# Kernel optimization log

Measured on AMD Instinct MI355X. Metric: run time of the kernel, lower is better.

## Reference

```python
import jax, jax.numpy as jnp
import numpy as np

B, L, D, H = 2, 2048, 1024, 16
HD = D // H
KW = 4  # conv kernel width


def layernorm(x, g, b, eps=1e-5):
    m = jnp.mean(x, axis=-1, keepdims=True)
    v = jnp.var(x, axis=-1, keepdims=True)
    return (x - m) / jnp.sqrt(v + eps) * g + b


def causal_conv(x, w, b):
    # torch Conv1d(k=4, padding=3, groups=D) then truncate to L => causal depthwise conv
    # out[t] = sum_j w[:, j] * x[t - 3 + j] + b
    xp = jnp.pad(x, ((0, 0), (KW - 1, 0), (0, 0)))
    Lx = x.shape[1]
    out = b
    for j in range(KW):
        out = out + xp[:, j:j + Lx, :] * w[:, j]
    return out


def setup_inputs() -> dict:
    key = jax.random.key(0)
    ks = jax.random.split(key, 16)
    r = lambda i, shape, s=0.02: jax.random.normal(ks[i], shape, jnp.float32) * s
    return dict(
        x=r(0, (B, L, D), 1.0),
        Wqkv=r(1, (D, 3 * D)), Wout=r(2, (D, D)),
        Wgate=r(3, (D, D)), bgate=jnp.zeros((D,), jnp.float32),
        fn_g=jnp.ones((D,), jnp.float32), fn_b=jnp.zeros((D,), jnp.float32),
        dn_g=jnp.ones((D,), jnp.float32), dn_b=jnp.zeros((D,), jnp.float32),
        dWq=r(4, (D, D)), dWk=r(5, (D, D)), dWv=r(6, (D, D)), dWo=r(7, (D, D)),
        Wbeta=r(8, (D, H)), bbeta=jnp.zeros((H,), jnp.float32),
        cq_w=r(9, (D, KW), 0.1), cq_b=jnp.zeros((D,), jnp.float32),
        ck_w=r(10, (D, KW), 0.1), ck_b=jnp.zeros((D,), jnp.float32),
        ln_g=jnp.ones((D,), jnp.float32), ln_b=jnp.zeros((D,), jnp.float32),
    )


def _delta_scan(q, k, v, beta):
    # q,k,v: (B,L,H,HD) ; beta: (B,L,H)
    Bx = q.shape[0]
    S0 = jnp.zeros((Bx, H, HD, HD), q.dtype)
    z0 = jnp.zeros((Bx, H, HD), q.dtype)

    def step(carry, inp):
        S, z = carry
        q_t, k_t, v_t, b_t = inp  # (B,H,HD) x3, (B,H)
        y = jnp.einsum('bhij,bhj->bhi', S, q_t)
        denom = jnp.einsum('bhi,bhi->bh', z, q_t)[..., None] + 1e-6
        y = y / denom
        old = jnp.einsum('bhij,bhj->bhi', S, k_t)
        delta = v_t - old
        S = S + b_t[..., None, None] * jnp.einsum('bhi,bhj->bhij', delta, k_t)
        z = z + b_t[..., None] * k_t
        return (S, z), y

    xs = (jnp.moveaxis(q, 1, 0), jnp.moveaxis(k, 1, 0),
          jnp.moveaxis(v, 1, 0), jnp.moveaxis(beta, 1, 0))
    (S, z), ys = jax.lax.scan(step, (S0, z0), xs)
    return jnp.moveaxis(ys, 0, 1), S, z  # (B,L,H,HD)


def _forward(x, Wqkv, Wout, Wgate, bgate, fn_g, fn_b, dn_g, dn_b,
             dWq, dWk, dWv, dWo, Wbeta, bbeta, cq_w, cq_b, ck_w, ck_b, ln_g, ln_b):
    Bx, Lx, Dx = x.shape
    # ---- flash (full causal, L<=2048 branch) ----
    qkv = (x @ Wqkv).reshape(Bx, Lx, 3, H, HD)
    q = jnp.moveaxis(qkv[:, :, 0], 1, 2)  # (B,H,L,HD)
    k = jnp.moveaxis(qkv[:, :, 1], 1, 2)
    v = jnp.moveaxis(qkv[:, :, 2], 1, 2)
    scale = HD ** -0.5
    scores = jnp.einsum('bhqd,bhkd->bhqk', q, k) * scale
    causal = jnp.tril(jnp.ones((Lx, Lx), bool))
    scores = jnp.where(causal, scores, -jnp.inf)
    attn = jax.nn.softmax(scores, axis=-1)
    flash = jnp.einsum('bhqk,bhkd->bhqd', attn, v)
    flash = jnp.moveaxis(flash, 1, 2).reshape(Bx, Lx, Dx) @ Wout
    flash = layernorm(flash, fn_g, fn_b)
    # ---- delta branch ----
    dq = causal_conv(x @ dWq, cq_w, cq_b).reshape(Bx, Lx, H, HD)
    dk = causal_conv(x @ dWk, ck_w, ck_b).reshape(Bx, Lx, H, HD)
    dv = (x @ dWv).reshape(Bx, Lx, H, HD)
    dk = dk / jnp.maximum(jnp.linalg.norm(dk, axis=-1, keepdims=True), 1e-12)
    beta = jax.nn.sigmoid(x @ Wbeta + bbeta)  # (B,L,H)
    ys, S, z = _delta_scan(dq, dk, dv, beta)
    delta_out = layernorm(ys.reshape(Bx, Lx, Dx) @ dWo, ln_g, ln_b)  # DeltaAttention layer_norm
    delta_out = layernorm(delta_out, dn_g, dn_b)  # hybrid delta_norm
    # ---- gate ----
    gate = jax.nn.sigmoid(x @ Wgate + bgate)
    out = gate * flash + (1.0 - gate) * delta_out
    return out, S, z


def reference(x, Wqkv, Wout, Wgate, bgate, fn_g, fn_b, dn_g, dn_b,
              dWq, dWk, dWv, dWo, Wbeta, bbeta, cq_w, cq_b, ck_w, ck_b, ln_g, ln_b):
    return _forward(x, Wqkv, Wout, Wgate, bgate, fn_g, fn_b, dn_g, dn_b,
                    dWq, dWk, dWv, dWo, Wbeta, bbeta, cq_w, cq_b, ck_w, ck_b, ln_g, ln_b)
```

## Files before the change

### kernel.cpp

```cpp
#include <hip/hip_runtime.h>
#include <hip/hip_bf16.h>

constexpr int B_ = 2, L_ = 2048, D_ = 1024, H_ = 16;

using bf16x8 = __attribute__((ext_vector_type(8))) short;
using f32x4  = __attribute__((ext_vector_type(4))) float;

__device__ __forceinline__ short f2b(float f) {
  union { float f; unsigned int u; } v; v.f = f;
  unsigned int r = (v.u + 0x7FFFu + ((v.u >> 16) & 1u)) >> 16;
  return (short)r;
}
__device__ __forceinline__ float b2f(unsigned short h) {
  union { unsigned int u; float f; } v; v.u = ((unsigned int)h) << 16; return v.f;
}
__device__ __forceinline__ void split2(float x, float y, unsigned int& h, unsigned int& l) {
  unsigned short hx = (unsigned short)f2b(x), hy = (unsigned short)f2b(y);
  h = (unsigned int)hx | ((unsigned int)hy << 16);
  unsigned short lx = (unsigned short)f2b(x - b2f(hx)), ly = (unsigned short)f2b(y - b2f(hy));
  l = (unsigned int)lx | ((unsigned int)ly << 16);
}
__device__ __forceinline__ float dot4(float4 a, float4 b) {
  return a.x * b.x + a.y * b.y + a.z * b.z + a.w * b.w;
}
// ... 116 lines not shown
    bf16x8 af[MT], bf[NT];
#pragma unroll
    for (int mt = 0; mt < MT; ++mt) af[mt] = *(bf16x8*)&As[(wm + mt * 16 + l15) * 32 + quad * 8];
#pragma unroll
    for (int nt = 0; nt < NT; ++nt) bf[nt] = *(bf16x8*)&Bs[(wn + nt * 16 + l15) * 32 + quad * 8];
#pragma unroll
    for (int mt = 0; mt < MT; ++mt)
#pragma unroll
      for (int nt = 0; nt < NT; ++nt)
        acc[mt][nt] = __builtin_amdgcn_mfma_f32_16x16x32_bf16(af[mt], bf[nt], acc[mt][nt], 0, 0, 0);
  }
#pragma unroll
  for (int mt = 0; mt < MT; ++mt)
#pragma unroll
    for (int nt = 0; nt < NT; ++nt)
#pragma unroll
      for (int r = 0; r < 4; ++r) {
        size_t idx = (size_t)(m0 + wm + mt * 16 + quad * 4 + r) * N + n0 + wn + nt * 16 + l15;
        if constexpr (sizeof(CT) == 2) C[idx] = f2b(acc[mt][nt][r]);
        else C[idx] = acc[mt][nt][r];
      }
}

template <int BN>
__global__ __launch_bounds__(256) void gemm_bt(const float* __restrict__ A, const short* __restrict__ Wt,
                                               float* __restrict__ C, int N, int K) {
  gemm_bt_body<BN, float>(A, Wt, C, N, K, blockIdx.x, blockIdx.y);
}

__global__ __launch_bounds__(256) void gemm_bt_h(const float* __restrict__ A, const short* __restrict__ Wt,
                                                 short* __restrict__ C, int N, int K) {
  gemm_bt_body<128, short>(A, Wt, C, N, K, blockIdx.x, blockIdx.y);
}

__global__ __launch_bounds__(256) void gemm_bt2(const float* __restrict__ A, const short* __restrict__ Wt1,
                                                const short* __restrict__ Wt2, float* __restrict__ C1,
                                                float* __restrict__ C2) {
  gemm_bt_body<64, float>(A, blockIdx.z ? Wt2 : Wt1, blockIdx.z ? C2 : C1, 1024, 1024,
                          blockIdx.x, blockIdx.y);
}

__global__ __launch_bounds__(256) void gemm_bt_split2(const float* __restrict__ A,
                                                      const short* __restrict__ Wh1, const short* __restrict__ Wl1,
                                                      const short* __restrict__ Wh2, const short* __restrict__ Wl2,
                                                      float* __restrict__ C1, float* __restrict__ C2) {
  constexpr int K = 1024, N = 1024;
  const short* Wh = blockIdx.z ? Wh2 : Wh1;
  const short* Wl = blockIdx.z ? Wl2 : Wl1;
  float* C = blockIdx.z ? C2 : C1;
  __shared__ __align__(16) short Ash[128 * 32];
  __shared__ __align__(16) short Asl[128 * 32];
  __shared__ __align__(16) short Bsh[64 * 32];
  __shared__ __align__(16) short Bsl[64 * 32];
  int tid = threadIdx.x;
  int wave = tid >> 6, lane = tid & 63, quad = lane >> 4, l15 = lane & 15;
  int m0 = blockIdx.y * 128, n0 = blockIdx.x * 64;
  int wm = wave * 32;
  f32x4 acc[2][4];
#pragma unroll
  for (int mt = 0; mt < 2; ++mt)
#pragma unroll
    for (int nt = 0; nt < 4; ++nt) acc[mt][nt] = (f32x4){0.f, 0.f, 0.f, 0.f};
// ... 35 lines not shown
    }
#pragma unroll
    for (int mt = 0; mt < 2; ++mt)
#pragma unroll
      for (int nt = 0; nt < 4; ++nt) {
        f32x4 a = acc[mt][nt];
        a = __builtin_amdgcn_mfma_f32_16x16x32_bf16(al[mt], bh[nt], a, 0, 0, 0);
        a = __builtin_amdgcn_mfma_f32_16x16x32_bf16(ah[mt], bl[nt], a, 0, 0, 0);
        a = __builtin_amdgcn_mfma_f32_16x16x32_bf16(ah[mt], bh[nt], a, 0, 0, 0);
        acc[mt][nt] = a;
      }
  }
#pragma unroll
  for (int mt = 0; mt < 2; ++mt)
#pragma unroll
    for (int nt = 0; nt < 4; ++nt)
#pragma unroll
      for (int r = 0; r < 4; ++r) {
        size_t idx = (size_t)(m0 + wm + mt * 16 + quad * 4 + r) * N + n0 + nt * 16 + l15;
        C[idx] = acc[mt][nt][r];
      }
}

__global__ __launch_bounds__(256) void attn_mfma(const short* __restrict__ qkv, float* __restrict__ outp) {
  __shared__ __align__(16) short Kl[64 * 64];
  __shared__ __align__(16) short Vt[64 * 64];
  __shared__ __align__(16) short Pl[64 * 64];
  int qb = 31 - blockIdx.x, h = blockIdx.y, b = blockIdx.z;
  int tid = threadIdx.x;
  int wave = tid >> 6, lane = tid & 63;
  int quad = lane >> 4, l15 = lane & 15;
  int qrow = qb * 64 + wave * 16 + l15;
  bf16x8 qf[2];
  {
    const short* qbase = qkv + (size_t)(b * L_ + qrow) * 3072 + h * 64;
#pragma unroll
    for (int s = 0; s < 2; ++s) qf[s] = *(const bf16x8*)(qbase + s * 32 + quad * 8);
  }
  f32x4 Of[4];
  float mrow[4], lrow[4], alpha[4];
#pragma unroll
  for (int dt = 0; dt < 4; ++dt) Of[dt] = (f32x4){0.f, 0.f, 0.f, 0.f};
#pragma unroll
  for (int r = 0; r < 4; ++r) { mrow[r] = -1e30f; lrow[r] = 0.f; }

  for (int kt = 0; kt <= qb; ++kt) {
    __syncthreads();
#pragma unroll
    for (int it = 0; it < 2; ++it) {
      int e8 = tid + it * 256;
      int key = e8 >> 3, g = e8 & 7;
      const short* src = qkv + ((size_t)((b * L_ + kt * 64 + key) * 3) + 1) * 1024 + h * 64 + g * 8;
      *(bf16x8*)&Kl[key * 64 + ((g ^ (key & 7)) << 3)] = *(const bf16x8*)src;
    }
    {
      int key4 = tid >> 4;
      int d4 = tid & 15;
      const short* vsrc = qkv + ((size_t)((b * L_ + kt * 64 + key4 * 4) * 3) + 2) * 1024 + h * 64 + d4 * 4;
      short4 v0 = *(const short4*)vsrc;
      short4 v1 = *(const short4*)(vsrc + 3072);
      short4 v2 = *(const short4*)(vsrc + 6144);
      short4 v3 = *(const short4*)(vsrc + 9216);
      short vr0[4] = {v0.x, v0.y, v0.z, v0.w};
      short vr1[4] = {v1.x, v1.y, v1.z, v1.w};
      short vr2[4] = {v2.x, v2.y, v2.z, v2.w};
      short vr3[4] = {v3.x, v3.y, v3.z, v3.w};
      int kg = key4 >> 1, k7b = (key4 & 1) * 4;
#pragma unroll
      for (int jj = 0; jj < 4; ++jj) {
        int d = d4 * 4 + jj;
        short4 sv;
        sv.x = vr0[jj]; sv.y = vr1[jj]; sv.z = vr2[jj]; sv.w = vr3[jj];
        *(short4*)&Vt[d * 64 + ((kg ^ (d & 7)) << 3) + k7b] = sv;
      }
    }
    __syncthreads();
    f32x4 sc[4];
#pragma unroll
    for (int nt = 0; nt < 4; ++nt) sc[nt] = (f32x4){0.f, 0.f, 0.f, 0.f};
#pragma unroll
    for (int s = 0; s < 2; ++s) {
#pragma unroll
      for (int nt = 0; nt < 4; ++nt) {
        int key = nt * 16 + l15;
        bf16x8 kf = *(bf16x8*)&Kl[key * 64 + (((4 * s + quad) ^ (key & 7)) << 3)];
        sc[nt] = __builtin_amdgcn_mfma_f32_16x16x32_bf16(qf[s], kf, sc[nt], 0, 0, 0);
      }
    }
    bool diag = (kt == qb);
#pragma unroll
    for (int r = 0; r < 4; ++r) {
      float sv[4];
#pragma unroll
      for (int nt = 0; nt < 4; ++nt) {
        float v = sc[nt][r] * 0.125f;
        if (diag && (nt * 16 + l15 > wave * 16 + quad * 4 + r)) v = -1e30f;
        sv[nt] = v;
      }
      float mx = fmaxf(fmaxf(sv[0], sv[1]), fmaxf(sv[2], sv[3]));
      mx = fmaxf(mx, __shfl_xor(mx, 1));
      mx = fmaxf(mx, __shfl_xor(mx, 2));
      mx = fmaxf(mx, __shfl_xor(mx, 4));
      mx = fmaxf(mx, __shfl_xor(mx, 8));
      float mnew = fmaxf(mrow[r], mx);
      float al = __expf(mrow[r] - mnew);
      mrow[r] = mnew;
      alpha[r] = al;
      int prow = wave * 16 + quad * 4 + r;
      int r7 = prow & 7;
      float ps = 0.f;
#pragma unroll
      for (int nt = 0; nt < 4; ++nt) {
        float p = __expf(sv[nt] - mnew);
        ps += p;
        Pl[prow * 64 + ((((nt << 1) + (l15 >> 3)) ^ r7) << 3) + (l15 & 7)] = f2b(p);
      }
      ps += __shfl_xor(ps, 1);
      ps += __shfl_xor(ps, 2);
      ps += __shfl_xor(ps, 4);
      ps += __shfl_xor(ps, 8);
      lrow[r] = lrow[r] * al + ps;
    }
#pragma unroll
    for (int dt = 0; dt < 4; ++dt)
#pragma unroll
      for (int r = 0; r < 4; ++r) Of[dt][r] *= alpha[r];
#pragma unroll
    for (int s = 0; s < 2; ++s) {
      bf16x8 pf = *(bf16x8*)&Pl[(wave * 16 + l15) * 64 + (((4 * s + quad) ^ (l15 & 7)) << 3)];
#pragma unroll
      for (int dt = 0; dt < 4; ++dt) {
        int d = dt * 16 + l15;
        bf16x8 vf = *(bf16x8*)&Vt[d * 64 + (((4 * s + quad) ^ (d & 7)) << 3)];
        Of[dt] = __builtin_amdgcn_mfma_f32_16x16x32_bf16(pf, vf, Of[dt], 0, 0, 0);
      }
    }
  }
#pragma unroll
  for (int r = 0; r < 4; ++r) alpha[r] = 1.f / lrow[r];
  int orow = qb * 64 + wave * 16 + quad * 4;
#pragma unroll
  for (int dt = 0; dt < 4; ++dt)
#pragma unroll
    for (int r = 0; r < 4; ++r)
      outp[(size_t)(b * L_ + orow + r) * 1024 + h * 64 + dt * 16 + l15] = Of[dt][r] * alpha[r];
}

__global__ __launch_bounds__(256) void ln_kernel(float* __restrict__ X, const float* __restrict__ g,
                                                 const float* __restrict__ bb) {
  int row = blockIdx.x, tid = threadIdx.x;
  float* xr = X + (size_t)row * D_;
  float v[4], s = 0.f, ss = 0.f;
#pragma unroll
  for (int i = 0; i < 4; ++i) { v[i] = xr[tid + i * 256]; s += v[i]; ss += v[i] * v[i]; }
#pragma unroll
  for (int off = 32; off; off >>= 1) { s += __shfl_xor(s, off); ss += __shfl_xor(ss, off); }
  __shared__ float rs[4], rss[4];
  if ((tid & 63) == 0) { rs[tid >> 6] = s; rss[tid >> 6] = ss; }
  __syncthreads();
  float S = rs[0] + rs[1] + rs[2] + rs[3];
  float SS = rss[0] + rss[1] + rss[2] + rss[3];
  float mean = S * (1.f / 1024.f);
  float var = SS * (1.f / 1024.f) - mean * mean;
  float inv = rsqrtf(var + 1e-5f);
#pragma unroll
  for (int i = 0; i < 4; ++i) {
    int c = tid + i * 256;
    xr[c] = (v[i] - mean) * inv * g[c] + bb[c];
  }
}

__global__ __launch_bounds__(256) void ln2mix_kernel(const float* __restrict__ X,
                                                     const float* __restrict__ g1, const float* __restrict__ b1,
                                                     const float* __restrict__ g2, const float* __restrict__ b2,
                                                     const float* __restrict__ gpre, const float* __restrict__ bgate,
                                                     const float* __restrict__ fo, float* __restrict__ outp) {
  int row = blockIdx.x, tid = threadIdx.x;
  const float* xr = X + (size_t)row * D_;
  __shared__ float rs[4], rss[4];
  float v[4], s = 0.f, ss = 0.f;
#pragma unroll
  for (int i = 0; i < 4; ++i) { v[i] = xr[tid + i * 256]; s += v[i]; ss += v[i] * v[i]; }
#pragma unroll
  for (int off = 32; off; off >>= 1) { s += __shfl_xor(s, off); ss += __shfl_xor(ss, off); }
  if ((tid & 63) == 0) { rs[tid >> 6] = s; rss[tid >> 6] = ss; }
  __syncthreads();
  float S = rs[0] + rs[1] + rs[2] + rs[3];
  float SS = rss[0] + rss[1] + rss[2] + rss[3];
  float mean = S * (1.f / 1024.f);
  float var = SS * (1.f / 1024.f) - mean * mean;
  float inv = rsqrtf(var + 1e-5f);
  s = 0.f; ss = 0.f;
#pragma unroll
  for (int i = 0; i < 4; ++i) {
    int c = tid + i * 256;
    v[i] = (v[i] - mean) * inv * g1[c] + b1[c];
    s += v[i]; ss += v[i] * v[i];
  }
#pragma unroll
  for (int off = 32; off; off >>= 1) { s += __shfl_xor(s, off); ss += __shfl_xor(ss, off); }
  __syncthreads();
  if ((tid & 63) == 0) { rs[tid >> 6] = s; rss[tid >> 6] = ss; }
  __syncthreads();
  S = rs[0] + rs[1] + rs[2] + rs[3];
  SS = rss[0] + rss[1] + rss[2] + rss[3];
  mean = S * (1.f / 1024.f);
  var = SS * (1.f / 1024.f) - mean * mean;
  inv = rsqrtf(var + 1e-5f);
#pragma unroll
  for (int i = 0; i < 4; ++i) {
    int c = tid + i * 256;
    size_t idx = (size_t)row * D_ + c;
    float w = (v[i] - mean) * inv * g2[c] + b2[c];
    float gg = 1.f / (1.f + __expf(-(gpre[idx] + bgate[c])));
    outp[idx] = gg * fo[idx] + (1.f - gg) * w;
  }
}

__global__ __launch_bounds__(256) void convnorm_kernel(const float* __restrict__ qin, const float* __restrict__ kin,
                                                       const float* __restrict__ qw, const float* __restrict__ qb,
                                                       const float* __restrict__ kw, const float* __restrict__ kb,
                                                       float* __restrict__ qout, float* __restrict__ kout) {
  int path = blockIdx.y;
  int row = blockIdx.x * 4 + (threadIdx.x >> 6);
  int lane = threadIdx.x & 63;
  int bl = row >> 4, h = row & 15;
  int t = bl & (L_ - 1);
  int d = h * 64 + lane;
  size_t idx = (size_t)bl * D_ + d;
  const float* xin = path ? kin : qin;
  const float* w = path ? kw : qw;
  const float* bias = path ? kb : qb;
  float acc = bias[d];
#pragma unroll
  for (int j = 0; j < 4; ++j) {
    int tt = t - 3 + j;
    if (tt >= 0) acc += w[d * 4 + j] * xin[idx + (size_t)(j - 3) * D_];
  }
// ... 112 lines not shown
      float4 x2 = *(float4*)&Xl[(u4 * 4 + 2) * 36 + s4];
      float4 x3 = *(float4*)&Xl[(u4 * 4 + 3) * 36 + s4];
      acc.x += bq.x * x0.x + bq.y * x1.x + bq.z * x2.x + bq.w * x3.x;
      acc.y += bq.x * x0.y + bq.y * x1.y + bq.z * x2.y + bq.w * x3.y;
      acc.z += bq.x * x0.z + bq.y * x1.z + bq.z * x2.z + bq.w * x3.z;
      acc.w += bq.x * x0.w + bq.y * x1.w + bq.z * x2.w + bq.w * x3.w;
    }
    *(float4*)&BqM_g[cb * 1024 + tt * 32 + s4] = acc;
  }
  if (tid < 32) {
    float a = 0.f;
#pragma unroll
    for (int s4i = 0; s4i < 8; ++s4i)
      a += dot4(*(float4*)&Bql[tid * 36 + s4i * 4], *(float4*)&bl[s4i * 4]);
    denB_g[cb * 32 + tid] = a;
  }
  if (tid >= 64 && tid < 128) {
    int j = tid - 64;
    float a = 0.f;
#pragma unroll
    for (int s = 0; s < 32; ++s) a += bl[s] * Kl[s * 68 + j];
    zinc_g[cb * 64 + j] = a;
  }
}

__global__ __launch_bounds__(256) void delta_kernel(const float* __restrict__ dq, const float* __restrict__ dk,
                                                    const float* __restrict__ dv, const float* __restrict__ beta,
                                                    const float* __restrict__ MK_g, const float* __restrict__ BqM_g,
                                                    const float* __restrict__ denB_g, const float* __restrict__ zinc_g,
                                                    float* __restrict__ ys, float* __restrict__ outS,
                                                    float* __restrict__ outZ) {
  __shared__ __align__(16) float MKl[2][32 * 68];
  __shared__ __align__(16) float BqMl[2][32 * 36];
  __shared__ __align__(16) float Vl[2][32 * 5];
  __shared__ __align__(16) float bll[2][32];
  __shared__ __align__(16) float dnl[2][32];
  __shared__ __align__(16) float zil[2][64];
  __shared__ __align__(16) float S0l[4 * 68];
  __shared__ __align__(16) float Y0l[32 * 5];
  __shared__ __align__(16) float Rtl[4 * 36];
  __shared__ __align__(16) float z0l[64];
  __shared__ __align__(16) float qzl[32];
  int bh = blockIdx.x & 31, grp = blockIdx.x >> 5;
  int b = bh >> 4, h = bh & 15;
  int i0 = grp * 4;
  int tid = threadIdx.x;
  int r = tid >> 3, j8 = (tid & 7) * 8;
  int js = tid & 7;
  size_t kqbase = (size_t)(b * L_) * 1024 + h * 64;

  for (int e = tid; e < 4 * 68; e += 256) S0l[e] = 0.f;
  if (tid < 64) z0l[tid] = 0.f;

  float4 kAc, kBc, qAc, qBc, kAn, kBn, qAn, qBn;
  float4 mA, mB, bqA, bqB;
  bqA = bqB = make_float4(0.f, 0.f, 0.f, 0.f);
  float vr = 0.f, blr = 0.f, dnb = 0.f, zi = 0.f;

#define KQLOAD(CN, KA, KB, QA, QB) { \
    size_t rb_ = kqbase + (size_t)((CN) * 32 + r) * 1024 + j8; \
    KA = ((const float4*)(dk + rb_))[0]; KB = ((const float4*)(dk + rb_))[1]; \
    QA = ((const float4*)(dq + rb_))[0]; QB = ((const float4*)(dq + rb_))[1]; \
  }
#define AUXLOAD(CN) { \
    size_t cb_ = (size_t)(bh * 64 + (CN)); \
    const float* mkp_ = MK_g + (cb_ * 32 + r) * 64 + j8; \
    mA = ((const float4*)mkp_)[0]; mB = ((const float4*)mkp_)[1]; \
    if (tid < 128) { \
      const float* bqp_ = BqM_g + cb_ * 1024 + (tid >> 2) * 32 + (tid & 3) * 8; \
      bqA = ((const float4*)bqp_)[0]; bqB = ((const float4*)bqp_)[1]; \
      vr = dv[(size_t)(b * L_ + (CN) * 32 + (tid >> 2)) * 1024 + h * 64 + i0 + (tid & 3)]; \
    } \
    if (tid < 32) { blr = beta[(size_t)(b * L_ + (CN) * 32 + tid) * 16 + h]; dnb = denB_g[cb_ * 32 + tid]; } \
    if (tid < 64) zi = zinc_g[cb_ * 64 + tid]; \
  }
#define AUXSTORE(NX) { \
    *(float4*)&MKl[NX][r * 68 + j8] = mA; *(float4*)&MKl[NX][r * 68 + j8 + 4] = mB; \
    if (tid < 128) { \
      int t_ = tid >> 2, s8_ = (tid & 3) * 8; \
      *(float4*)&BqMl[NX][t_ * 36 + s8_] = bqA; \
      *(float4*)&BqMl[NX][t_ * 36 + s8_ + 4] = bqB; \
      Vl[NX][t_ * 5 + (tid & 3)] = vr; \
    } \
    if (tid < 32) { bll[NX][tid] = blr; dnl[NX][tid] = dnb; } \
    if (tid < 64) zil[NX][tid] = zi; \
  }

  KQLOAD(0, kAc, kBc, qAc, qBc);
  AUXLOAD(0);
  AUXSTORE(0);
  __syncthreads();

  for (int c = 0; c < 64; ++c) {
    int cur = c & 1, nxt = cur ^ 1;
    int cn = (c + 1 < 64) ? c + 1 : 63;
    KQLOAD(cn, kAn, kBn, qAn, qBn);
    AUXLOAD(cn);
    {
      float aK[4], aY[4];
#pragma unroll
      for (int i = 0; i < 4; ++i) {
        float4 s0 = *(float4*)&S0l[i * 68 + j8];
        float4 s1 = *(float4*)&S0l[i * 68 + j8 + 4];
        aK[i] = dot4(kAc, s0) + dot4(kBc, s1);
        aY[i] = dot4(qAc, s0) + dot4(qBc, s1);
      }
      float4 z0 = *(float4*)&z0l[j8];
      float4 z1 = *(float4*)&z0l[j8 + 4];
      float aZ = dot4(qAc, z0) + dot4(qBc, z1);
#pragma unroll
      for (int off = 1; off <= 4; off <<= 1) {
#pragma unroll
        for (int i = 0; i < 4; ++i) {
          aK[i] += __shfl_xor(aK[i], off);
          aY[i] += __shfl_xor(aY[i], off);
        }
        aZ += __shfl_xor(aZ, off);
      }
      if (js == 0) {
        float be = bll[cur][r];
#pragma unroll
        for (int i = 0; i < 4; ++i) {
          Rtl[i * 36 + r] = be * (Vl[cur][r * 5 + i] - aK[i]);
          Y0l[r * 5 + i] = aY[i];
        }
        qzl[r] = aZ;
      }
    }
    __syncthreads();
    if (tid < 128) {
      int i2 = tid >> 5;
      int j2 = (tid & 31) * 2;
      float a0 = S0l[i2 * 68 + j2];
      float a1 = S0l[i2 * 68 + j2 + 1];
#pragma unroll
      for (int s4i = 0; s4i < 8; ++s4i) {
        float4 rt = *(float4*)&Rtl[i2 * 36 + s4i * 4];
        float2 m0 = *(float2*)&MKl[cur][(s4i * 4 + 0) * 68 + j2];
        float2 m1 = *(float2*)&MKl[cur][(s4i * 4 + 1) * 68 + j2];
        float2 m2 = *(float2*)&MKl[cur][(s4i * 4 + 2) * 68 + j2];
        float2 m3 = *(float2*)&MKl[cur][(s4i * 4 + 3) * 68 + j2];
        a0 += rt.x * m0.x + rt.y * m1.x + rt.z * m2.x + rt.w * m3.x;
        a1 += rt.x * m0.y + rt.y * m1.y + rt.z * m2.y + rt.w * m3.y;
      }
      S0l[i2 * 68 + j2] = a0;
      S0l[i2 * 68 + j2 + 1] = a1;
      if (tid < 64) z0l[tid] += zil[cur][tid];
    } else {
      int t = (tid >> 2) & 31;
      int i = tid & 3;
      float acc = Y0l[t * 5 + i];
#pragma unroll
      for (int s4i = 0; s4i < 8; ++s4i)
        acc += dot4(*(float4*)&BqMl[cur][t * 36 + s4i * 4], *(float4*)&Rtl[i * 36 + s4i * 4]);
      float y = acc / (qzl[t] + dnl[cur][t] + 1e-6f);
      ys[(size_t)(b * L_ + c * 32 + t) * 1024 + h * 64 + i0 + i] = y;
    }
    AUXSTORE(nxt);
    kAc = kAn; kBc = kBn; qAc = qAn; qBc = qBn;
    __syncthreads();
  }
#undef KQLOAD
#undef AUXLOAD
#undef AUXSTORE
  {
    int i = tid >> 6, j = tid & 63;
    outS[((size_t)(bh * 64) + i0 + i) * 64 + j] = S0l[i * 68 + j];
  }
  if (grp == 0 && tid < 64) outZ[bh * 64 + tid] = z0l[tid];
}

extern "C" void kernel_launch(void* const* d_in, const int* in_sizes, int n_in,
                              void* d_out, int out_size, void* d_ws, size_t ws_size,
                              hipStream_t stream) {
  const float* x     = (const float*)d_in[0];
  const float* Wqkv  = (const float*)d_in[1];
  const float* Wout  = (const float*)d_in[2];
  const float* Wgate = (const float*)d_in[3];
  const float* bgate = (const float*)d_in[4];
  const float* fn_g  = (const float*)d_in[5];
  const float* fn_b  = (const float*)d_in[6];
  const float* dn_g  = (const float*)d_in[7];
  const float* dn_b  = (const float*)d_in[8];
  const float* dWq   = (const float*)d_in[9];
  const float* dWk   = (const float*)d_in[10];
  const float* dWv   = (const float*)d_in[11];
  const float* dWo   = (const float*)d_in[12];
  const float* Wbeta = (const float*)d_in[13];
  const float* bbeta = (const float*)d_in[14];
  const float* cq_w  = (const float*)d_in[15];
  const float* cq_b  = (const float*)d_in[16];
  const float* ck_w  = (const float*)d_in[17];
  const float* ck_b  = (const float*)d_in[18];
  const float* ln_g  = (const float*)d_in[19];
  const float* ln_b  = (const float*)d_in[20];

  float* ws = (float*)d_ws;
  short* qkvh   = (short*)ws;
  float* dv     = ws;
  float* dqc    = ws + 4194304;
  float* dkc    = ws + 8388608;
  float* attnO  = ws + 12582912;
  short* wtg    = (short*)(ws + 12582912);
  short* Wvt    = (short*)(ws + 14680064);
  float* denB_g = ws + 12582912;
  float* zinc_g = ws + 12582912 + 65536;
  float* BqM_g  = ws + 14680064;
  float* do1    = ws + 12582912;
  float* fo     = ws + 16777216;
  float* dqp    = ws + 20971520;
  float* gpre   = ws + 20971520;
  float* dkp    = ws + 25165824;
  float* MK_g   = ws + 25165824;
  float* betab  = ws + 29360128;

  short* Wqkvt = (short*)(ws + 20971520);
  short* Woutt = (short*)(ws + 29426688);
  short* Wot   = (short*)(ws + 4194304);

  short* Wqh = (short*)(ws + 8388608);
  short* Wql = (short*)(ws + 8912896);
  short* Wkh = (short*)(ws + 9437184);
  short* Wkl = (short*)(ws + 9961472);

  float* out  = (float*)d_out;
  float* outS = out + 4194304;
  float* outZ = out + 4325376;
  float* ysb  = out;

  tcast<<<dim3(48, 16), 256, 0, stream>>>(Wqkv, Wqkvt, 3072, 1024);
  gemm_bt_h<<<dim3(24, 32), 256, 0, stream>>>(x, Wqkvt, qkvh, 3072, 1024);
  attn_mfma<<<dim3(32, H_, B_), 256, 0, stream>>>(qkvh, attnO);
  tcast<<<dim3(16, 16), 256, 0, stream>>>(Wout, Woutt, 1024, 1024);
  gemm_bt<64><<<dim3(16, 32), 256, 0, stream>>>(attnO, Woutt, fo, 1024, 1024);
  ln_kernel<<<4096, 256, 0, stream>>>(fo, fn_g, fn_b);
  tcast_split2<<<dim3(16, 16, 2), 256, 0, stream>>>(dWq, dWk, Wqh, Wql, Wkh, Wkl);
  gemm_bt_split2<<<dim3(16, 32, 2), 256, 0, stream>>>(x, Wqh, Wql, Wkh, Wkl, dqp, dkp);
  convnorm_kernel<<<dim3(16384, 2), 256, 0, stream>>>(dqp, dkp, cq_w, cq_b, ck_w, ck_b, dqc, dkc);
  beta_kernel<<<4096, 256, 0, stream>>>(x, Wbeta, bbeta, betab);
  tcast2<<<dim3(16, 16, 2), 256, 0, stream>>>(dWv, Wgate, Wvt, wtg);
  gemm_bt2<<<dim3(16, 32, 2), 256, 0, stream>>>(x, Wvt, wtg, dv, gpre);
  prep_kernel<<<dim3(64, 32), 256, 0, stream>>>(dqc, dkc, betab, MK_g, BqM_g, denB_g, zinc_g);
  delta_kernel<<<512, 256, 0, stream>>>(dqc, dkc, dv, betab, MK_g, BqM_g, denB_g, zinc_g, ysb, outS, outZ);
  tcast<<<dim3(16, 16), 256, 0, stream>>>(dWo, Wot, 1024, 1024);
  gemm_bt<64><<<dim3(16, 32), 256, 0, stream>>>(ysb, Wot, do1, 1024, 1024);
  ln2mix_kernel<<<4096, 256, 0, stream>>>(do1, ln_g, ln_b, dn_g, dn_b, gpre, bgate, fo, out);
}
```

Baseline: 750.4 us.

## Co-schedule attention and delta scan in one launch, batch output GEMMs, fuse flash layernorm

Merges the flash attention kernel and the sequential delta-scan kernel into one launch: 512 delta blocks are followed by 1024 attention blocks, sharing overlaid shared memory. The aim is for attention work to fill the GPU while the few long-running delta blocks serialise. Attention and delta outputs are now stored as bf16, so the two output projections can run as one batched bf16-A GEMM. The flash layernorm is folded into the final mix kernel. This removes several launches and fp32 round trips, at the cost of bf16 rounding of the intermediate activations and a more complex workspace aliasing plan.

```diff
diff --git a/kernel.cpp b/kernel.cpp
--- a/kernel.cpp
+++ b/kernel.cpp
@@ -162,12 +162,6 @@
       }
 }
 
-template <int BN>
-__global__ __launch_bounds__(256) void gemm_bt(const float* __restrict__ A, const short* __restrict__ Wt,
-                                               float* __restrict__ C, int N, int K) {
-  gemm_bt_body<BN, float>(A, Wt, C, N, K, blockIdx.x, blockIdx.y);
-}
-
 __global__ __launch_bounds__(256) void gemm_bt_h(const float* __restrict__ A, const short* __restrict__ Wt,
                                                  short* __restrict__ C, int N, int K) {
   gemm_bt_body<128, short>(A, Wt, C, N, K, blockIdx.x, blockIdx.y);
@@ -178,6 +172,59 @@
                                                 float* __restrict__ C2) {
   gemm_bt_body<64, float>(A, blockIdx.z ? Wt2 : Wt1, blockIdx.z ? C2 : C1, 1024, 1024,
                           blockIdx.x, blockIdx.y);
+}
+
+__global__ __launch_bounds__(256) void gemm_bt2_hA(const short* __restrict__ A1, const short* __restrict__ Wt1,
+                                                   const short* __restrict__ A2, const short* __restrict__ Wt2,
+                                                   float* __restrict__ C1, float* __restrict__ C2) {
+  constexpr int K = 1024, N = 1024;
+  const short* A = blockIdx.z ? A2 : A1;
+  const short* Wt = blockIdx.z ? Wt2 : Wt1;
+  float* C = blockIdx.z ? C2 : C1;
+  __shared__ __align__(16) short As[128 * 32];
+  __shared__ __align__(16) short Bs[64 * 32];
+  int tid = threadIdx.x;
+  int wave = tid >> 6, lane = tid & 63, quad = lane >> 4, l15 = lane & 15;
+  int m0 = blockIdx.y * 128, n0 = blockIdx.x * 64;
+  int wm = wave * 32;
+  f32x4 acc[2][4];
+#pragma unroll
+  for (int mt = 0; mt < 2; ++mt)
+#pragma unroll
+    for (int nt = 0; nt < 4; ++nt) acc[mt][nt] = (f32x4){0.f, 0.f, 0.f, 0.f};
+  for (int k0 = 0; k0 < K; k0 += 32) {
+    __syncthreads();
+#pragma unroll
+    for (int i = 0; i < 2; ++i) {
+      int chunk = i * 256 + tid;
+      int m = chunk >> 2, kc = (chunk & 3) * 8;
+      *(uint4*)&As[m * 32 + kc] = *(const uint4*)(A + (size_t)(m0 + m) * K + k0 + kc);
+    }
+    {
+      int n = tid >> 2, kc = (tid & 3) * 8;
+      *(uint4*)&Bs[n * 32 + kc] = *(const uint4*)(Wt + (size_t)(n0 + n) * K + k0 + kc);
+    }
+    __syncthreads();
+    bf16x8 af[2], bf[4];
+#pragma unroll
+    for (int mt = 0; mt < 2; ++mt) af[mt] = *(bf16x8*)&As[(wm + mt * 16 + l15) * 32 + quad * 8];
+#pragma unroll
+    for (int nt = 0; nt < 4; ++nt) bf[nt] = *(bf16x8*)&Bs[(nt * 16 + l15) * 32 + quad * 8];
+#pragma unroll
+    for (int mt = 0; mt < 2; ++mt)
+#pragma unroll
+      for (int nt = 0; nt < 4; ++nt)
+        acc[mt][nt] = __builtin_amdgcn_mfma_f32_16x16x32_bf16(af[mt], bf[nt], acc[mt][nt], 0, 0, 0);
+  }
+#pragma unroll
+  for (int mt = 0; mt < 2; ++mt)
+#pragma unroll
+    for (int nt = 0; nt < 4; ++nt)
+#pragma unroll
+      for (int r = 0; r < 4; ++r) {
+        size_t idx = (size_t)(m0 + wm + mt * 16 + quad * 4 + r) * N + n0 + nt * 16 + l15;
+        C[idx] = acc[mt][nt][r];
+      }
 }
 
 __global__ __launch_bounds__(256) void gemm_bt_split2(const float* __restrict__ A,
@@ -259,11 +306,166 @@
       }
 }
 
-__global__ __launch_bounds__(256) void attn_mfma(const short* __restrict__ qkv, float* __restrict__ outp) {
-  __shared__ __align__(16) short Kl[64 * 64];
-  __shared__ __align__(16) short Vt[64 * 64];
-  __shared__ __align__(16) short Pl[64 * 64];
-  int qb = 31 - blockIdx.x, h = blockIdx.y, b = blockIdx.z;
+struct DeltaSmem {
+  float MKl[2][32 * 68];
+  float BqMl[2][32 * 36];
+  float Vl[2][32 * 5];
+  float bll[2][32];
+  float dnl[2][32];
+  float zil[2][64];
+  float S0l[4 * 68];
+  float Y0l[32 * 5];
+  float Rtl[4 * 36];
+  float z0l[64];
+  float qzl[32];
+};
+struct AttnSmem {
+  short Kl[64 * 64];
+  short Vt[64 * 64];
+  short Pl[64 * 64];
+};
+
+__device__ __forceinline__ void delta_body(char* smraw, int bidx,
+                                           const float* __restrict__ dq, const float* __restrict__ dk,
+                                           const float* __restrict__ dv, const float* __restrict__ beta,
+                                           const float* __restrict__ MK_g, const float* __restrict__ BqM_g,
+                                           const float* __restrict__ denB_g, const float* __restrict__ zinc_g,
+                                           short* __restrict__ ys_h, float* __restrict__ outS,
+                                           float* __restrict__ outZ) {
+  DeltaSmem& sm = *reinterpret_cast<DeltaSmem*>(smraw);
+  int bh = bidx & 31, grp = bidx >> 5;
+  int b = bh >> 4, h = bh & 15;
+  int i0 = grp * 4;
+  int tid = threadIdx.x;
+  int r = tid >> 3, j8 = (tid & 7) * 8;
+  int js = tid & 7;
+  size_t kqbase = (size_t)(b * L_) * 1024 + h * 64;
+
+  for (int e = tid; e < 4 * 68; e += 256) sm.S0l[e] = 0.f;
+  if (tid < 64) sm.z0l[tid] = 0.f;
+
+  float4 kAc, kBc, qAc, qBc, kAn, kBn, qAn, qBn;
+  float4 mA, mB, bqA, bqB;
+  bqA = bqB = make_float4(0.f, 0.f, 0.f, 0.f);
+  float vr = 0.f, blr = 0.f, dnb = 0.f, zi = 0.f;
+
+#define KQLOAD(CN, KA, KB, QA, QB) { \
+    size_t rb_ = kqbase + (size_t)((CN) * 32 + r) * 1024 + j8; \
+    KA = ((const float4*)(dk + rb_))[0]; KB = ((const float4*)(dk + rb_))[1]; \
+    QA = ((const float4*)(dq + rb_))[0]; QB = ((const float4*)(dq + rb_))[1]; \
+  }
+#define AUXLOAD(CN) { \
+    size_t cb_ = (size_t)(bh * 64 + (CN)); \
+    const float* mkp_ = MK_g + (cb_ * 32 + r) * 64 + j8; \
+    mA = ((const float4*)mkp_)[0]; mB = ((const float4*)mkp_)[1]; \
+    if (tid < 128) { \
+      const float* bqp_ = BqM_g + cb_ * 1024 + (tid >> 2) * 32 + (tid & 3) * 8; \
+      bqA = ((const float4*)bqp_)[0]; bqB = ((const float4*)bqp_)[1]; \
+      vr = dv[(size_t)(b * L_ + (CN) * 32 + (tid >> 2)) * 1024 + h * 64 + i0 + (tid & 3)]; \
+    } \
+    if (tid < 32) { blr = beta[(size_t)(b * L_ + (CN) * 32 + tid) * 16 + h]; dnb = denB_g[cb_ * 32 + tid]; } \
+    if (tid < 64) zi = zinc_g[cb_ * 64 + tid]; \
+  }
+#define AUXSTORE(NX) { \
+    *(float4*)&sm.MKl[NX][r * 68 + j8] = mA; *(float4*)&sm.MKl[NX][r * 68 + j8 + 4] = mB; \
+    if (tid < 128) { \
+      int t_ = tid >> 2, s8_ = (tid & 3) * 8; \
+      *(float4*)&sm.BqMl[NX][t_ * 36 + s8_] = bqA; \
+      *(float4*)&sm.BqMl[NX][t_ * 36 + s8_ + 4] = bqB; \
+      sm.Vl[NX][t_ * 5 + (tid & 3)] = vr; \
+    } \
+    if (tid < 32) { sm.bll[NX][tid] = blr; sm.dnl[NX][tid] = dnb; } \
+    if (tid < 64) sm.zil[NX][tid] = zi; \
+  }
+
+  KQLOAD(0, kAc, kBc, qAc, qBc);
+  AUXLOAD(0);
+  AUXSTORE(0);
+  __syncthreads();
+
+  for (int c = 0; c < 64; ++c) {
+    int cur = c & 1, nxt = cur ^ 1;
+    int cn = (c + 1 < 64) ? c + 1 : 63;
+    KQLOAD(cn, kAn, kBn, qAn, qBn);
+    AUXLOAD(cn);
+    {
+      float aK[4], aY[4];
+#pragma unroll
+      for (int i = 0; i < 4; ++i) {
+        float4 s0 = *(float4*)&sm.S0l[i * 68 + j8];
+        float4 s1 = *(float4*)&sm.S0l[i * 68 + j8 + 4];
+        aK[i] = dot4(kAc, s0) + dot4(kBc, s1);
+        aY[i] = dot4(qAc, s0) + dot4(qBc, s1);
+      }
+      float4 z0 = *(float4*)&sm.z0l[j8];
+      float4 z1 = *(float4*)&sm.z0l[j8 + 4];
+      float aZ = dot4(qAc, z0) + dot4(qBc, z1);
+#pragma unroll
+      for (int off = 1; off <= 4; off <<= 1) {
+#pragma unroll
+        for (int i = 0; i < 4; ++i) {
+          aK[i] += __shfl_xor(aK[i], off);
+          aY[i] += __shfl_xor(aY[i], off);
+        }
+        aZ += __shfl_xor(aZ, off);
+      }
+      if (js == 0) {
+        float be = sm.bll[cur][r];
+#pragma unroll
+        for (int i = 0; i < 4; ++i) {
+          sm.Rtl[i * 36 + r] = be * (sm.Vl[cur][r * 5 + i] - aK[i]);
+          sm.Y0l[r * 5 + i] = aY[i];
+        }
+        sm.qzl[r] = aZ;
+      }
+    }
+    __syncthreads();
+    if (tid < 128) {
+      int i2 = tid >> 5;
+      int j2 = (tid & 31) * 2;
+      float a0 = sm.S0l[i2 * 68 + j2];
+      float a1 = sm.S0l[i2 * 68 + j2 + 1];
+#pragma unroll
+      for (int s4i = 0; s4i < 8; ++s4i) {
+        float4 rt = *(float4*)&sm.Rtl[i2 * 36 + s4i * 4];
+        float2 m0 = *(float2*)&sm.MKl[cur][(s4i * 4 + 0) * 68 + j2];
+        float2 m1 = *(float2*)&sm.MKl[cur][(s4i * 4 + 1) * 68 + j2];
+        float2 m2 = *(float2*)&sm.MKl[cur][(s4i * 4 + 2) * 68 + j2];
+        float2 m3 = *(float2*)&sm.MKl[cur][(s4i * 4 + 3) * 68 + j2];
+        a0 += rt.x * m0.x + rt.y * m1.x + rt.z * m2.x + rt.w * m3.x;
+        a1 += rt.x * m0.y + rt.y * m1.y + rt.z * m2.y + rt.w * m3.y;
+      }
+      sm.S0l[i2 * 68 + j2] = a0;
+      sm.S0l[i2 * 68 + j2 + 1] = a1;
+      if (tid < 64) sm.z0l[tid] += sm.zil[cur][tid];
+    } else {
+      int t = (tid >> 2) & 31;
+      int i = tid & 3;
+      float acc = sm.Y0l[t * 5 + i];
+#pragma unroll
+      for (int s4i = 0; s4i < 8; ++s4i)
+        acc += dot4(*(float4*)&sm.BqMl[cur][t * 36 + s4i * 4], *(float4*)&sm.Rtl[i * 36 + s4i * 4]);
+      float y = acc / (sm.qzl[t] + sm.dnl[cur][t] + 1e-6f);
+      ys_h[(size_t)(b * L_ + c * 32 + t) * 1024 + h * 64 + i0 + i] = f2b(y);
+    }
+    AUXSTORE(nxt);
+    kAc = kAn; kBc = kBn; qAc = qAn; qBc = qBn;
+    __syncthreads();
+  }
+#undef KQLOAD
+#undef AUXLOAD
+#undef AUXSTORE
+  {
+    int i = tid >> 6, j = tid & 63;
+    outS[((size_t)(bh * 64) + i0 + i) * 64 + j] = sm.S0l[i * 68 + j];
+  }
+  if (grp == 0 && tid < 64) outZ[bh * 64 + tid] = sm.z0l[tid];
+}
+
+__device__ __forceinline__ void attn_body(char* smraw, int idx, const short* __restrict__ qkv,
+                                          short* __restrict__ outp_h) {
+  AttnSmem& sm = *reinterpret_cast<AttnSmem*>(smraw);
+  int qb = 31 - (idx & 31), h = (idx >> 5) & 15, b = idx >> 9;
   int tid = threadIdx.x;
   int wave = tid >> 6, lane = tid & 63;
   int quad = lane >> 4, l15 = lane & 15;
@@ -288,7 +490,7 @@
       int e8 = tid + it * 256;
       int key = e8 >> 3, g = e8 & 7;
       const short* src = qkv + ((size_t)((b * L_ + kt * 64 + key) * 3) + 1) * 1024 + h * 64 + g * 8;
-      *(bf16x8*)&Kl[key * 64 + ((g ^ (key & 7)) << 3)] = *(const bf16x8*)src;
+      *(bf16x8*)&sm.Kl[key * 64 + ((g ^ (key & 7)) << 3)] = *(const bf16x8*)src;
     }
     {
       int key4 = tid >> 4;
@@ -308,7 +510,7 @@
         int d = d4 * 4 + jj;
         short4 sv;
         sv.x = vr0[jj]; sv.y = vr1[jj]; sv.z = vr2[jj]; sv.w = vr3[jj];
-        *(short4*)&Vt[d * 64 + ((kg ^ (d & 7)) << 3) + k7b] = sv;
+        *(short4*)&sm.Vt[d * 64 + ((kg ^ (d & 7)) << 3) + k7b] = sv;
       }
     }
     __syncthreads();
@@ -320,7 +522,7 @@
 #pragma unroll
       for (int nt = 0; nt < 4; ++nt) {
         int key = nt * 16 + l15;
-        bf16x8 kf = *(bf16x8*)&Kl[key * 64 + (((4 * s + quad) ^ (key & 7)) << 3)];
+        bf16x8 kf = *(bf16x8*)&sm.Kl[key * 64 + (((4 * s + quad) ^ (key & 7)) << 3)];
         sc[nt] = __builtin_amdgcn_mfma_f32_16x16x32_bf16(qf[s], kf, sc[nt], 0, 0, 0);
       }
     }
@@ -350,7 +552,7 @@
       for (int nt = 0; nt < 4; ++nt) {
         float p = __expf(sv[nt] - mnew);
         ps += p;
-        Pl[prow * 64 + ((((nt << 1) + (l15 >> 3)) ^ r7) << 3) + (l15 & 7)] = f2b(p);
+        sm.Pl[prow * 64 + ((((nt << 1) + (l15 >> 3)) ^ r7) << 3) + (l15 & 7)] = f2b(p);
       }
       ps += __shfl_xor(ps, 1);
       ps += __shfl_xor(ps, 2);
@@ -364,11 +566,11 @@
       for (int r = 0; r < 4; ++r) Of[dt][r] *= alpha[r];
 #pragma unroll
     for (int s = 0; s < 2; ++s) {
-      bf16x8 pf = *(bf16x8*)&Pl[(wave * 16 + l15) * 64 + (((4 * s + quad) ^ (l15 & 7)) << 3)];
+      bf16x8 pf = *(bf16x8*)&sm.Pl[(wave * 16 + l15) * 64 + (((4 * s + quad) ^ (l15 & 7)) << 3)];
 #pragma unroll
       for (int dt = 0; dt < 4; ++dt) {
         int d = dt * 16 + l15;
-        bf16x8 vf = *(bf16x8*)&Vt[d * 64 + (((4 * s + quad) ^ (d & 7)) << 3)];
+        bf16x8 vf = *(bf16x8*)&sm.Vt[d * 64 + (((4 * s + quad) ^ (d & 7)) << 3)];
         Of[dt] = __builtin_amdgcn_mfma_f32_16x16x32_bf16(pf, vf, Of[dt], 0, 0, 0);
       }
     }
@@ -380,53 +582,59 @@
   for (int dt = 0; dt < 4; ++dt)
 #pragma unroll
     for (int r = 0; r < 4; ++r)
-      outp[(size_t)(b * L_ + orow + r) * 1024 + h * 64 + dt * 16 + l15] = Of[dt][r] * alpha[r];
-}
-
-__global__ __launch_bounds__(256) void ln_kernel(float* __restrict__ X, const float* __restrict__ g,
-                                                 const float* __restrict__ bb) {
+      outp_h[(size_t)(b * L_ + orow + r) * 1024 + h * 64 + dt * 16 + l15] = f2b(Of[dt][r] * alpha[r]);
+}
+
+__global__ __launch_bounds__(256) void attn_delta_fused(
+    const short* __restrict__ qkv, short* __restrict__ attnO_h,
+    const float* __restrict__ dq, const float* __restrict__ dk,
+    const float* __restrict__ dv, const float* __restrict__ beta,
+    const float* __restrict__ MK_g, const float* __restrict__ BqM_g,
+    const float* __restrict__ denB_g, const float* __restrict__ zinc_g,
+    short* __restrict__ ys_h, float* __restrict__ outS, float* __restrict__ outZ) {
+  __shared__ __align__(16) char smem[sizeof(DeltaSmem)];
+  static_assert(sizeof(DeltaSmem) >= sizeof(AttnSmem), "overlay");
+  if (blockIdx.x < 512)
+    delta_body(smem, blockIdx.x, dq, dk, dv, beta, MK_g, BqM_g, denB_g, zinc_g, ys_h, outS, outZ);
+  else
+    attn_body(smem, blockIdx.x - 512, qkv, attnO_h);
+}
+
+__global__ __launch_bounds__(256) void ln2mix_f(const float* __restrict__ X,
+                                                const float* __restrict__ g1, const float* __restrict__ b1,
+                                                const float* __restrict__ g2, const float* __restrict__ b2,
+                                                const float* __restrict__ gpre, const float* __restrict__ bgate,
+                                                const float* __restrict__ foraw,
+                                                const float* __restrict__ fng, const float* __restrict__ fnb,
+                                                float* __restrict__ outp) {
   int row = blockIdx.x, tid = threadIdx.x;
-  float* xr = X + (size_t)row * D_;
-  float v[4], s = 0.f, ss = 0.f;
-#pragma unroll
-  for (int i = 0; i < 4; ++i) { v[i] = xr[tid + i * 256]; s += v[i]; ss += v[i] * v[i]; }
-#pragma unroll
-  for (int off = 32; off; off >>= 1) { s += __shfl_xor(s, off); ss += __shfl_xor(ss, off); }
-  __shared__ float rs[4], rss[4];
-  if ((tid & 63) == 0) { rs[tid >> 6] = s; rss[tid >> 6] = ss; }
+  const float* xr = X + (size_t)row * D_;
+  const float* fr = foraw + (size_t)row * D_;
+  __shared__ float rs[4], rss[4], frs[4], frss[4];
+  float v[4], f[4];
+  float s = 0.f, ss = 0.f, fs = 0.f, fss = 0.f;
+#pragma unroll
+  for (int i = 0; i < 4; ++i) {
+    v[i] = xr[tid + i * 256]; s += v[i]; ss += v[i] * v[i];
+    f[i] = fr[tid + i * 256]; fs += f[i]; fss += f[i] * f[i];
+  }
+#pragma unroll
+  for (int off = 32; off; off >>= 1) {
+    s += __shfl_xor(s, off); ss += __shfl_xor(ss, off);
+    fs += __shfl_xor(fs, off); fss += __shfl_xor(fss, off);
+  }
+  if ((tid & 63) == 0) { rs[tid >> 6] = s; rss[tid >> 6] = ss; frs[tid >> 6] = fs; frss[tid >> 6] = fss; }
   __syncthreads();
   float S = rs[0] + rs[1] + rs[2] + rs[3];
   float SS = rss[0] + rss[1] + rss[2] + rss[3];
+  float FS = frs[0] + frs[1] + frs[2] + frs[3];
+  float FSS = frss[0] + frss[1] + frss[2] + frss[3];
   float mean = S * (1.f / 1024.f);
   float var = SS * (1.f / 1024.f) - mean * mean;
   float inv = rsqrtf(var + 1e-5f);
-#pragma unroll
-  for (int i = 0; i < 4; ++i) {
-    int c = tid + i * 256;
-    xr[c] = (v[i] - mean) * inv * g[c] + bb[c];
-  }
-}
-
-__global__ __launch_bounds__(256) void ln2mix_kernel(const float* __restrict__ X,
-                                                     const float* __restrict__ g1, const float* __restrict__ b1,
-                                                     const float* __restrict__ g2, const float* __restrict__ b2,
-                                                     const float* __restrict__ gpre, const float* __restrict__ bgate,
-                                                     const float* __restrict__ fo, float* __restrict__ outp) {
-  int row = blockIdx.x, tid = threadIdx.x;
-  const float* xr = X + (size_t)row * D_;
-  __shared__ float rs[4], rss[4];
-  float v[4], s = 0.f, ss = 0.f;
-#pragma unroll
-  for (int i = 0; i < 4; ++i) { v[i] = xr[tid + i * 256]; s += v[i]; ss += v[i] * v[i]; }
-#pragma unroll
-  for (int off = 32; off; off >>= 1) { s += __shfl_xor(s, off); ss += __shfl_xor(ss, off); }
-  if ((tid & 63) == 0) { rs[tid >> 6] = s; rss[tid >> 6] = ss; }
-  __syncthreads();
-  float S = rs[0] + rs[1] + rs[2] + rs[3];
-  float SS = rss[0] + rss[1] + rss[2] + rss[3];
-  float mean = S * (1.f / 1024.f);
-  float var = SS * (1.f / 1024.f) - mean * mean;
-  float inv = rsqrtf(var + 1e-5f);
+  float fmean = FS * (1.f / 1024.f);
+  float fvar = FSS * (1.f / 1024.f) - fmean * fmean;
+  float finv = rsqrtf(fvar + 1e-5f);
   s = 0.f; ss = 0.f;
 #pragma unroll
   for (int i = 0; i < 4; ++i) {
@@ -449,8 +657,9 @@
     int c = tid + i * 256;
     size_t idx = (size_t)row * D_ + c;
     float w = (v[i] - mean) * inv * g2[c] + b2[c];
+    float fl = (f[i] - fmean) * finv * fng[c] + fnb[c];
     float gg = 1.f / (1.f + __expf(-(gpre[idx] + bgate[c])));
-    outp[idx] = gg * fo[idx] + (1.f - gg) * w;
+    outp[idx] = gg * fl + (1.f - gg) * w;
   }
 }
 
@@ -609,152 +818,6 @@
     for (int s = 0; s < 32; ++s) a += bl[s] * Kl[s * 68 + j];
     zinc_g[cb * 64 + j] = a;
   }
-}
-
-__global__ __launch_bounds__(256) void delta_kernel(const float* __restrict__ dq, const float* __restrict__ dk,
-                                                    const float* __restrict__ dv, const float* __restrict__ beta,
-                                                    const float* __restrict__ MK_g, const float* __restrict__ BqM_g,
-                                                    const float* __restrict__ denB_g, const float* __restrict__ zinc_g,
-                                                    float* __restrict__ ys, float* __restrict__ outS,
-                                                    float* __restrict__ outZ) {
-  __shared__ __align__(16) float MKl[2][32 * 68];
-  __shared__ __align__(16) float BqMl[2][32 * 36];
-  __shared__ __align__(16) float Vl[2][32 * 5];
-  __shared__ __align__(16) float bll[2][32];
-  __shared__ __align__(16) float dnl[2][32];
-  __shared__ __align__(16) float zil[2][64];
-  __shared__ __align__(16) float S0l[4 * 68];
-  __shared__ __align__(16) float Y0l[32 * 5];
-  __shared__ __align__(16) float Rtl[4 * 36];
-  __shared__ __align__(16) float z0l[64];
-  __shared__ __align__(16) float qzl[32];
-  int bh = blockIdx.x & 31, grp = blockIdx.x >> 5;
-  int b = bh >> 4, h = bh & 15;
-  int i0 = grp * 4;
-  int tid = threadIdx.x;
-  int r = tid >> 3, j8 = (tid & 7) * 8;
-  int js = tid & 7;
-  size_t kqbase = (size_t)(b * L_) * 1024 + h * 64;
-
-  for (int e = tid; e < 4 * 68; e += 256) S0l[e] = 0.f;
-  if (tid < 64) z0l[tid] = 0.f;
-
-  float4 kAc, kBc, qAc, qBc, kAn, kBn, qAn, qBn;
-  float4 mA, mB, bqA, bqB;
-  bqA = bqB = make_float4(0.f, 0.f, 0.f, 0.f);
-  float vr = 0.f, blr = 0.f, dnb = 0.f, zi = 0.f;
-
-#define KQLOAD(CN, KA, KB, QA, QB) { \
-    size_t rb_ = kqbase + (size_t)((CN) * 32 + r) * 1024 + j8; \
-    KA = ((const float4*)(dk + rb_))[0]; KB = ((const float4*)(dk + rb_))[1]; \
-    QA = ((const float4*)(dq + rb_))[0]; QB = ((const float4*)(dq + rb_))[1]; \
-  }
-#define AUXLOAD(CN) { \
-    size_t cb_ = (size_t)(bh * 64 + (CN)); \
-    const float* mkp_ = MK_g + (cb_ * 32 + r) * 64 + j8; \
-    mA = ((const float4*)mkp_)[0]; mB = ((const float4*)mkp_)[1]; \
-    if (tid < 128) { \
-      const float* bqp_ = BqM_g + cb_ * 1024 + (tid >> 2) * 32 + (tid & 3) * 8; \
-      bqA = ((const float4*)bqp_)[0]; bqB = ((const float4*)bqp_)[1]; \
-      vr = dv[(size_t)(b * L_ + (CN) * 32 + (tid >> 2)) * 1024 + h * 64 + i0 + (tid & 3)]; \
-    } \
-    if (tid < 32) { blr = beta[(size_t)(b * L_ + (CN) * 32 + tid) * 16 + h]; dnb = denB_g[cb_ * 32 + tid]; } \
-    if (tid < 64) zi = zinc_g[cb_ * 64 + tid]; \
-  }
-#define AUXSTORE(NX) { \
-    *(float4*)&MKl[NX][r * 68 + j8] = mA; *(float4*)&MKl[NX][r * 68 + j8 + 4] = mB; \
-    if (tid < 128) { \
-      int t_ = tid >> 2, s8_ = (tid & 3) * 8; \
-      *(float4*)&BqMl[NX][t_ * 36 + s8_] = bqA; \
-      *(float4*)&BqMl[NX][t_ * 36 + s8_ + 4] = bqB; \
-      Vl[NX][t_ * 5 + (tid & 3)] = vr; \
-    } \
-    if (tid < 32) { bll[NX][tid] = blr; dnl[NX][tid] = dnb; } \
-    if (tid < 64) zil[NX][tid] = zi; \
-  }
-
-  KQLOAD(0, kAc, kBc, qAc, qBc);
-  AUXLOAD(0);
-  AUXSTORE(0);
-  __syncthreads();
-
-  for (int c = 0; c < 64; ++c) {
-    int cur = c & 1, nxt = cur ^ 1;
-    int cn = (c + 1 < 64) ? c + 1 : 63;
-    KQLOAD(cn, kAn, kBn, qAn, qBn);
-    AUXLOAD(cn);
-    {
-      float aK[4], aY[4];
-#pragma unroll
-      for (int i = 0; i < 4; ++i) {
-        float4 s0 = *(float4*)&S0l[i * 68 + j8];
-        float4 s1 = *(float4*)&S0l[i * 68 + j8 + 4];
-        aK[i] = dot4(kAc, s0) + dot4(kBc, s1);
-        aY[i] = dot4(qAc, s0) + dot4(qBc, s1);
-      }
-      float4 z0 = *(float4*)&z0l[j8];
-      float4 z1 = *(float4*)&z0l[j8 + 4];
-      float aZ = dot4(qAc, z0) + dot4(qBc, z1);
-#pragma unroll
-      for (int off = 1; off <= 4; off <<= 1) {
-#pragma unroll
-        for (int i = 0; i < 4; ++i) {
-          aK[i] += __shfl_xor(aK[i], off);
-          aY[i] += __shfl_xor(aY[i], off);
-        }
-        aZ += __shfl_xor(aZ, off);
-      }
-      if (js == 0) {
-        float be = bll[cur][r];
-#pragma unroll
-        for (int i = 0; i < 4; ++i) {
-          Rtl[i * 36 + r] = be * (Vl[cur][r * 5 + i] - aK[i]);
-          Y0l[r * 5 + i] = aY[i];
-        }
-        qzl[r] = aZ;
-      }
-    }
-    __syncthreads();
-    if (tid < 128) {
-      int i2 = tid >> 5;
-      int j2 = (tid & 31) * 2;
-      float a0 = S0l[i2 * 68 + j2];
-      float a1 = S0l[i2 * 68 + j2 + 1];
-#pragma unroll
-      for (int s4i = 0; s4i < 8; ++s4i) {
-        float4 rt = *(float4*)&Rtl[i2 * 36 + s4i * 4];
-        float2 m0 = *(float2*)&MKl[cur][(s4i * 4 + 0) * 68 + j2];
-        float2 m1 = *(float2*)&MKl[cur][(s4i * 4 + 1) * 68 + j2];
-        float2 m2 = *(float2*)&MKl[cur][(s4i * 4 + 2) * 68 + j2];
-        float2 m3 = *(float2*)&MKl[cur][(s4i * 4 + 3) * 68 + j2];
-        a0 += rt.x * m0.x + rt.y * m1.x + rt.z * m2.x + rt.w * m3.x;
-        a1 += rt.x * m0.y + rt.y * m1.y + rt.z * m2.y + rt.w * m3.y;
-      }
-      S0l[i2 * 68 + j2] = a0;
-      S0l[i2 * 68 + j2 + 1] = a1;
-      if (tid < 64) z0l[tid] += zil[cur][tid];
-    } else {
-      int t = (tid >> 2) & 31;
-      int i = tid & 3;
-      float acc = Y0l[t * 5 + i];
-#pragma unroll
-      for (int s4i = 0; s4i < 8; ++s4i)
-        acc += dot4(*(float4*)&BqMl[cur][t * 36 + s4i * 4], *(float4*)&Rtl[i * 36 + s4i * 4]);
-      float y = acc / (qzl[t] + dnl[cur][t] + 1e-6f);
-      ys[(size_t)(b * L_ + c * 32 + t) * 1024 + h * 64 + i0 + i] = y;
-    }
-    AUXSTORE(nxt);
-    kAc = kAn; kBc = kBn; qAc = qAn; qBc = qBn;
-    __syncthreads();
-  }
-#undef KQLOAD
-#undef AUXLOAD
-#undef AUXSTORE
-  {
-    int i = tid >> 6, j = tid & 63;
-    outS[((size_t)(bh * 64) + i0 + i) * 64 + j] = S0l[i * 68 + j];
-  }
-  if (grp == 0 && tid < 64) outZ[bh * 64 + tid] = z0l[tid];
 }
 
 extern "C" void kernel_launch(void* const* d_in, const int* in_sizes, int n_in,
@@ -783,53 +846,48 @@
   const float* ln_b  = (const float*)d_in[20];
 
   float* ws = (float*)d_ws;
-  short* qkvh   = (short*)ws;
-  float* dv     = ws;
-  float* dqc    = ws + 4194304;
-  float* dkc    = ws + 8388608;
-  float* attnO  = ws + 12582912;
-  short* wtg    = (short*)(ws + 12582912);
-  short* Wvt    = (short*)(ws + 14680064);
-  float* denB_g = ws + 12582912;
-  float* zinc_g = ws + 12582912 + 65536;
-  float* BqM_g  = ws + 14680064;
-  float* do1    = ws + 12582912;
-  float* fo     = ws + 16777216;
-  float* dqp    = ws + 20971520;
-  float* gpre   = ws + 20971520;
-  float* dkp    = ws + 25165824;
-  float* MK_g   = ws + 25165824;
-  float* betab  = ws + 29360128;
-
-  short* Wqkvt = (short*)(ws + 20971520);
-  short* Woutt = (short*)(ws + 29426688);
-  short* Wot   = (short*)(ws + 4194304);
-
-  short* Wqh = (short*)(ws + 8388608);
-  short* Wql = (short*)(ws + 8912896);
-  short* Wkh = (short*)(ws + 9437184);
-  short* Wkl = (short*)(ws + 9961472);
+  float* dqc    = ws;
+  float* dkc    = ws + 4194304;
+  float* dv     = ws + 8388608;
+  float* gpre   = ws + 12582912;
+  float* MK_g   = ws + 16777216;
+  float* BqM_g  = ws + 20971520;
+  float* denB_g = ws + 23068672;
+  float* zinc_g = ws + 23134208;
+  float* betab  = ws + 23265280;
+  short* qkvh   = (short*)(ws + 23330816);
+  short* Wqh = (short*)(ws + 16777216);
+  short* Wql = (short*)(ws + 17301504);
+  short* Wkh = (short*)(ws + 17825792);
+  short* Wkl = (short*)(ws + 18350080);
+  float* dqp = ws + 18874368;
+  float* dkp = ws + 23330816;
+  short* Wvt = (short*)(ws + 16777216);
+  short* wtg = (short*)(ws + 17301504);
+  short* Wqkvt = (short*)(ws + 16777216);
+  short* Woutt = (short*)(ws + 4194304);
+  short* Wot   = (short*)(ws + 4718592);
+  float* fo    = ws + 16777216;
+  float* do1   = ws + 8388608;
 
   float* out  = (float*)d_out;
   float* outS = out + 4194304;
   float* outZ = out + 4325376;
-  float* ysb  = out;
-
-  tcast<<<dim3(48, 16), 256, 0, stream>>>(Wqkv, Wqkvt, 3072, 1024);
-  gemm_bt_h<<<dim3(24, 32), 256, 0, stream>>>(x, Wqkvt, qkvh, 3072, 1024);
-  attn_mfma<<<dim3(32, H_, B_), 256, 0, stream>>>(qkvh, attnO);
-  tcast<<<dim3(16, 16), 256, 0, stream>>>(Wout, Woutt, 1024, 1024);
-  gemm_bt<64><<<dim3(16, 32), 256, 0, stream>>>(attnO, Woutt, fo, 1024, 1024);
-  ln_kernel<<<4096, 256, 0, stream>>>(fo, fn_g, fn_b);
+  short* ysb_h   = (short*)out;
+  short* attnO_h = (short*)(out + 2097152);
+
   tcast_split2<<<dim3(16, 16, 2), 256, 0, stream>>>(dWq, dWk, Wqh, Wql, Wkh, Wkl);
   gemm_bt_split2<<<dim3(16, 32, 2), 256, 0, stream>>>(x, Wqh, Wql, Wkh, Wkl, dqp, dkp);
   convnorm_kernel<<<dim3(16384, 2), 256, 0, stream>>>(dqp, dkp, cq_w, cq_b, ck_w, ck_b, dqc, dkc);
   beta_kernel<<<4096, 256, 0, stream>>>(x, Wbeta, bbeta, betab);
   tcast2<<<dim3(16, 16, 2), 256, 0, stream>>>(dWv, Wgate, Wvt, wtg);
   gemm_bt2<<<dim3(16, 32, 2), 256, 0, stream>>>(x, Wvt, wtg, dv, gpre);
+  tcast<<<dim3(48, 16), 256, 0, stream>>>(Wqkv, Wqkvt, 3072, 1024);
+  gemm_bt_h<<<dim3(24, 32), 256, 0, stream>>>(x, Wqkvt, qkvh, 3072, 1024);
   prep_kernel<<<dim3(64, 32), 256, 0, stream>>>(dqc, dkc, betab, MK_g, BqM_g, denB_g, zinc_g);
-  delta_kernel<<<512, 256, 0, stream>>>(dqc, dkc, dv, betab, MK_g, BqM_g, denB_g, zinc_g, ysb, outS, outZ);
-  tcast<<<dim3(16, 16), 256, 0, stream>>>(dWo, Wot, 1024, 1024);
-  gemm_bt<64><<<dim3(16, 32), 256, 0, stream>>>(ysb, Wot, do1, 1024, 1024);
-  ln2mix_kernel<<<4096, 256, 0, stream>>>(do1, ln_g, ln_b, dn_g, dn_b, gpre, bgate, fo, out);
-}
+  attn_delta_fused<<<1536, 256, 0, stream>>>(qkvh, attnO_h, dqc, dkc, dv, betab,
+                                             MK_g, BqM_g, denB_g, zinc_g, ysb_h, outS, outZ);
+  tcast2<<<dim3(16, 16, 2), 256, 0, stream>>>(Wout, dWo, Woutt, Wot);
+  gemm_bt2_hA<<<dim3(16, 32, 2), 256, 0, stream>>>(attnO_h, Woutt, ysb_h, Wot, fo, do1);
+  ln2mix_f<<<4096, 256, 0, stream>>>(do1, ln_g, ln_b, dn_g, dn_b, gpre, bgate, fo, fn_g, fn_b, out);
+}
```

Result: faster. 701.7 us (-6.5%).
